# Kernel optimization log

Hardware: AMD Instinct MI355X
Metric: run time of the kernel (lower is better)

## Reference

```python
import jax, jax.numpy as jnp
import numpy as np

N_EMB = 1024
HEAD_SIZE = 128


def setup_inputs() -> dict:
    key = jax.random.key(0)
    k1, k2, k3, k4 = jax.random.split(key, 4)
    B, T = 8, 4096
    x = jax.random.normal(k1, (B, T, N_EMB), dtype=jnp.float32)
    # nn.Linear(n_emb, head_size, bias=False) weights have shape [head_size, n_emb]
    s = 1.0 / np.sqrt(N_EMB)
    Wq = jax.random.uniform(k2, (HEAD_SIZE, N_EMB), jnp.float32, -s, s)
    Wk = jax.random.uniform(k3, (HEAD_SIZE, N_EMB), jnp.float32, -s, s)
    Wv = jax.random.uniform(k4, (HEAD_SIZE, N_EMB), jnp.float32, -s, s)
    return {"x": x, "Wq": Wq, "Wk": Wk, "Wv": Wv}


def reference(x, Wq, Wk, Wv):
    # x: [B, T, C]; W*: [H, C]
    B, T, C = x.shape
    H = Wq.shape[0]
    q = jnp.einsum('btc,hc->bth', x, Wq)
    k = jnp.einsum('btc,hc->bth', x, Wk)
    v = jnp.einsum('btc,hc->bth', x, Wv)
    scale = H ** -0.5
    wei = jnp.einsum('bth,bsh->bts', q, k) * scale  # [B, T, T]
    # causal mask: position t attends to s <= t
    causal = jnp.arange(T)[:, None] >= jnp.arange(T)[None, :]
    wei = jnp.where(causal, wei, -jnp.inf)
    wei = jax.nn.softmax(wei, axis=-1)
    # dropout treated as identity (eval mode)
    out = jnp.einsum('bts,bsh->bth', wei, v)  # [B, T, H]
    return out
```

## Files before the change

### kernel.cpp

```cpp
#include <hip/hip_runtime.h>
#include <hip/hip_bf16.h>

typedef __bf16 bf16_t;
typedef __attribute__((ext_vector_type(8))) __bf16 bf16x8;
typedef __attribute__((ext_vector_type(4))) __bf16 bf16x4;
typedef __attribute__((ext_vector_type(4))) float f32x4;

#define MFMA16(a, b, c) __builtin_amdgcn_mfma_f32_16x16x32_bf16((a), (b), (c), 0, 0, 0)

__device__ __forceinline__ void gload_lds16(const void* g, void* l) {
    __builtin_amdgcn_global_load_lds(
        (const __attribute__((address_space(1))) void*)g,
        (__attribute__((address_space(3))) void*)l, 16, 0, 0);
}

__global__ __launch_bounds__(256, 3) void proj_qkv(
    const float* __restrict__ X,
    const float* __restrict__ W0, const float* __restrict__ W1, const float* __restrict__ W2,
    bf16_t* __restrict__ O0, bf16_t* __restrict__ O1, bf16_t* __restrict__ O2)
{
    __shared__ __align__(16) char As[128 * 128];
    __shared__ __align__(16) char Bs[128 * 128];

    const int tid = threadIdx.x;
    const int wid = tid >> 6;
    const int lane = tid & 63;
    const int l15 = lane & 15, l4 = lane >> 4;
    const int wr = wid >> 1, wc = wid & 1;
    const int m0 = blockIdx.x * 128;

    const float* W = (blockIdx.y == 0) ? W0 : (blockIdx.y == 1 ? W1 : W2);

    const int r0 = tid >> 4;
    const int kq = tid & 15;
    const int swz = ((r0 & 7) << 4);

    f32x4 acc[4][4] = {};
    float4 xr[8];

    #pragma unroll
    for (int i = 0; i < 8; ++i)
        xr[i] = *(const float4*)(X + (size_t)(m0 + r0 + i * 16) * 1024 + kq * 4);

    for (int ks = 0; ks < 16; ++ks) {
        const int kb = ks * 64;
        #pragma unroll
        for (int i = 0; i < 8; ++i) {
            const int r = r0 + i * 16;
            bf16x4 av; av[0] = (bf16_t)xr[i].x; av[1] = (bf16_t)xr[i].y;
            av[2] = (bf16_t)xr[i].z; av[3] = (bf16_t)xr[i].w;
            *(bf16x4*)(As + r * 128 + ((kq * 8) ^ swz)) = av;
        }
        #pragma unroll
        for (int i = 0; i < 8; ++i) {
            const int r = r0 + i * 16;
            float4 wa = *(const float4*)(W + (size_t)r * 1024 + kb + kq * 4);
            bf16x4 wv; wv[0] = (bf16_t)wa.x; wv[1] = (bf16_t)wa.y;
            wv[2] = (bf16_t)wa.z; wv[3] = (bf16_t)wa.w;
            *(bf16x4*)(Bs + r * 128 + ((kq * 8) ^ swz)) = wv;
        }
        __syncthreads();
        if (ks < 15) {
            #pragma unroll
            for (int i = 0; i < 8; ++i)
                xr[i] = *(const float4*)(X + (size_t)(m0 + r0 + i * 16) * 1024 + kb + 64 + kq * 4);
        }
        #pragma unroll
        for (int kk = 0; kk < 64; kk += 32) {
            const int kbyte = 2 * kk + 16 * l4;
            bf16x8 af[4], bfr[4];
            #pragma unroll
            for (int mi = 0; mi < 4; ++mi) {
                int r = wr * 64 + mi * 16 + l15;
                af[mi] = *(const bf16x8*)(As + r * 128 + (kbyte ^ ((r & 7) << 4)));
            }
            #pragma unroll
            for (int ni = 0; ni < 4; ++ni) {
                int r = wc * 64 + ni * 16 + l15;
                bfr[ni] = *(const bf16x8*)(Bs + r * 128 + (kbyte ^ ((r & 7) << 4)));
            }
            #pragma unroll
            for (int mi = 0; mi < 4; ++mi)
                #pragma unroll
                for (int ni = 0; ni < 4; ++ni)
                    acc[mi][ni] = MFMA16(af[mi], bfr[ni], acc[mi][ni]);
        }
        __syncthreads();
    }

    if (blockIdx.y < 2) {
        const float sc = (blockIdx.y == 0) ? 0.12751754816f : 1.0f;
        bf16_t* O = (blockIdx.y == 0) ? O0 : O1;
        #pragma unroll
        for (int mi = 0; mi < 4; ++mi)
            #pragma unroll
            for (int ni = 0; ni < 4; ++ni) {
                int row = m0 + wr * 64 + mi * 16 + l4 * 4;
                int col = wc * 64 + ni * 16 + l15;
                #pragma unroll
                for (int r = 0; r < 4; ++r)
                    O[(size_t)(row + r) * 128 + col] = (bf16_t)(acc[mi][ni][r] * sc);
            }
    } else {
        #pragma unroll
        for (int mi = 0; mi < 4; ++mi)
            #pragma unroll
            for (int ni = 0; ni < 4; ++ni) {
                int row0 = m0 + wr * 64 + mi * 16 + l4 * 4;
                int col = wc * 64 + ni * 16 + l15;
                int bb = row0 >> 12, t0 = row0 & 4095;
                bf16x4 pk;
                #pragma unroll
                for (int r = 0; r < 4; ++r) pk[r] = (bf16_t)acc[mi][ni][r];
                *(bf16x4*)(O2 + ((size_t)bb << 19) + (size_t)col * 4096 + t0) = pk;
            }
    }
}

__global__ __launch_bounds__(256, 2) void attn_fwd(
    const bf16_t* __restrict__ Qb, const bf16_t* __restrict__ Kb,
    const bf16_t* __restrict__ Vtg, float* __restrict__ out, int Bn)
{
    __shared__ __align__(16) char lds[81920];

    const int tid = threadIdx.x, wid = tid >> 6, lane = tid & 63;
    const int l15 = lane & 15, l4 = lane >> 4;
    const int pair = wid >> 1, qhalf = wid & 1;

    const int L = blockIdx.x;
    const int b = L % Bn;
    const int j = L / Bn;
    const int qt = (j < 32) ? j : 95 - j;
    const int q0 = qt << 6;
    const int steps = (qt >> 1) + 1;
    const int qw0 = q0 + 32 * qhalf;

    const size_t base = (size_t)b * 4096 * 128;

    bf16x8 aq[2][4];
    #pragma unroll
    for (int qs = 0; qs < 2; ++qs)
        #pragma unroll
        for (int kf = 0; kf < 4; ++kf)
            aq[qs][kf] = *(const bf16x8*)(Qb + base + (size_t)(qw0 + 16 * qs + l15) * 128 + 32 * kf + 8 * l4);

    float mx[2] = {-1e30f, -1e30f}, lsum[2] = {0.f, 0.f};
    f32x4 o[2][8] = {};

    char* Kbuf = lds + pair * 32768;
    char* Vbuf = Kbuf + 16384;
    char* Pw   = lds + 65536 + wid * 4096;
    char* stg  = lds + wid * 16384;

    const int sK_r = lane >> 4, sK_c = (lane & 15) << 4;
    const int sV_r = lane >> 3, sV_c = (lane & 7) << 4;

    auto stage = [&](int s) {
        const int t = 2 * s + pair;
        if (t * 64 > q0 + 63) return;
        const int kv0s = t << 6;
        if ((wid & 1) == 0) {
            #pragma unroll
            for (int i = 0; i < 16; ++i) {
                const int row = i * 4 + sK_r;
                const bf16_t* src = Kb + base + (size_t)(kv0s + row) * 128
                                    + ((sK_c ^ ((row & 7) << 4)) >> 1);
                gload_lds16(src, stg + i * 1024);
            }
        } else {
            #pragma unroll
            for (int i = 0; i < 16; ++i) {
                const int h = i * 8 + sV_r;
                const bf16_t* src = Vtg + base + (size_t)h * 4096 + kv0s
                                    + ((sV_c ^ ((h & 7) << 4)) >> 1);
                gload_lds16(src, stg + i * 1024);
            }
        }
    };

    stage(0);
    __syncthreads();

    for (int s = 0; s < steps; ++s) {
        const int tw = 2 * s + pair;
        const int kv0 = tw << 6;
        if (kv0 <= qw0 + 31) {
            f32x4 sa[2][4];
            #pragma unroll
            for (int qs = 0; qs < 2; ++qs)
                #pragma unroll
                for (int ni = 0; ni < 4; ++ni) sa[qs][ni] = (f32x4){0.f, 0.f, 0.f, 0.f};
            __builtin_amdgcn_s_setprio(1);
            #pragma unroll
            for (int kf = 0; kf < 4; ++kf) {
                const int kb = 64 * kf + 16 * l4;
                #pragma unroll
                for (int ni = 0; ni < 4; ++ni) {
                    const int krow = 16 * ni + l15;
                    bf16x8 ak = *(const bf16x8*)(Kbuf + krow * 256 + (kb ^ ((krow & 7) << 4)));
                    sa[0][ni] = MFMA16(ak, aq[0][kf], sa[0][ni]);
                    sa[1][ni] = MFMA16(ak, aq[1][kf], sa[1][ni]);
                }
            }
            __builtin_amdgcn_s_setprio(0);
            #pragma unroll
            for (int qs = 0; qs < 2; ++qs) {
                const int qg = qw0 + 16 * qs + l15;
                if (kv0 + 63 > qw0 + 16 * qs) {
                    #pragma unroll
                    for (int ni = 0; ni < 4; ++ni)
                        #pragma unroll
                        for (int r = 0; r < 4; ++r)
                            if (kv0 + 16 * ni + 4 * l4 + r > qg) sa[qs][ni][r] = -1e30f;
                }
                float tm = sa[qs][0][0];
                #pragma unroll
                for (int ni = 0; ni < 4; ++ni)
                    #pragma unroll
                    for (int r = 0; r < 4; ++r) tm = fmaxf(tm, sa[qs][ni][r]);
                tm = fmaxf(tm, __shfl_xor(tm, 16, 64));
                tm = fmaxf(tm, __shfl_xor(tm, 32, 64));
                const float mnew = fmaxf(mx[qs], tm);
                const float c = exp2f(mx[qs] - mnew);
                float ssum = 0.f;
                #pragma unroll
                for (int ni = 0; ni < 4; ++ni)
                    #pragma unroll
                    for (int r = 0; r < 4; ++r) {
                        float pv = exp2f(sa[qs][ni][r] - mnew);
                        sa[qs][ni][r] = pv;
                        ssum += pv;
                    }
                ssum += __shfl_xor(ssum, 16, 64);
                ssum += __shfl_xor(ssum, 32, 64);
                lsum[qs] = lsum[qs] * c + ssum;
                mx[qs] = mnew;
                #pragma unroll
                for (int mf = 0; mf < 8; ++mf) {
                    f32x4 t = o[qs][mf];
                    t[0] *= c; t[1] *= c; t[2] *= c; t[3] *= c;
                    o[qs][mf] = t;
                }
                const int rowb = (16 * qs + l15) * 128;
                const int swz = (l15 & 7) << 4;
                #pragma unroll
                for (int ni = 0; ni < 4; ++ni) {
                    bf16x4 pv;
                    pv[0] = (bf16_t)sa[qs][ni][0]; pv[1] = (bf16_t)sa[qs][ni][1];
                    pv[2] = (bf16_t)sa[qs][ni][2]; pv[3] = (bf16_t)sa[qs][ni][3];
                    *(bf16x4*)(Pw + rowb + ((32 * ni + 8 * l4) ^ swz)) = pv;
                }
            }
            const int swzp = (l15 & 7) << 4;
            __builtin_amdgcn_s_setprio(1);
            #pragma unroll
            for (int kfp = 0; kfp < 2; ++kfp) {
                const int kb = 64 * kfp + 16 * l4;
                bf16x8 p0 = *(const bf16x8*)(Pw + l15 * 128 + (kb ^ swzp));
                bf16x8 p1 = *(const bf16x8*)(Pw + (16 + l15) * 128 + (kb ^ swzp));
                #pragma unroll
                for (int mf = 0; mf < 8; ++mf) {
                    const int h = 16 * mf + l15;
                    bf16x8 av = *(const bf16x8*)(Vbuf + h * 128 + (kb ^ ((h & 7) << 4)));
                    o[0][mf] = MFMA16(av, p0, o[0][mf]);
                    o[1][mf] = MFMA16(av, p1, o[1][mf]);
                }
            }
            __builtin_amdgcn_s_setprio(0);
        }
        if (s + 1 < steps) {
            __syncthreads();
            stage(s + 1);
            __syncthreads();
        }
    }

    __syncthreads();
    if (wid >= 2) {
        char* dst = lds + (wid - 2) * 16384;
        #pragma unroll
        for (int qs = 0; qs < 2; ++qs)
            #pragma unroll
            for (int mf = 0; mf < 8; ++mf)
                *(f32x4*)(dst + (qs * 8 + mf) * 1024 + lane * 16) = o[qs][mf];
        f32x4 st; st[0] = mx[0]; st[1] = lsum[0]; st[2] = mx[1]; st[3] = lsum[1];
        *(f32x4*)(lds + 32768 + (wid - 2) * 1024 + lane * 16) = st;
    }
    __syncthreads();
    if (wid < 2) {
        char* srcO = lds + wid * 16384;
        f32x4 st = *(const f32x4*)(lds + 32768 + wid * 1024 + lane * 16);
        #pragma unroll
        for (int qs = 0; qs < 2; ++qs) {
            const float mB = st[2 * qs], lB = st[2 * qs + 1];
            const float mm = fmaxf(mx[qs], mB);
            const float a = exp2f(mx[qs] - mm), bb = exp2f(mB - mm);
            const float linv = 1.f / (lsum[qs] * a + lB * bb);
            const int qg = qw0 + 16 * qs + l15;
            float* op = out + ((size_t)b * 4096 + qg) * 128;
            #pragma unroll
            for (int mf = 0; mf < 8; ++mf) {
                f32x4 ob = *(const f32x4*)(srcO + (qs * 8 + mf) * 1024 + lane * 16);
                f32x4 r;
                #pragma unroll
                for (int e = 0; e < 4; ++e) r[e] = (o[qs][mf][e] * a + ob[e] * bb) * linv;
                *(f32x4*)(op + 16 * mf + 4 * l4) = r;
            }
        }
    }
}

extern "C" void kernel_launch(void* const* d_in, const int* in_sizes, int n_in,
                              void* d_out, int out_size, void* d_ws, size_t ws_size,
                              hipStream_t stream) {
    const float* X  = (const float*)d_in[0];
    const float* Wq = (const float*)d_in[1];
    const float* Wk = (const float*)d_in[2];
    const float* Wv = (const float*)d_in[3];
    float* out = (float*)d_out;

    const int M = in_sizes[0] / 1024;
    const int Bn = M / 4096;

    bf16_t* Qb  = (bf16_t*)d_ws;
    bf16_t* KbP = Qb + (size_t)M * 128;
    bf16_t* VtP = KbP + (size_t)M * 128;

    proj_qkv<<<dim3(M / 128, 3), 256, 0, stream>>>(X, Wq, Wk, Wv, Qb, KbP, VtP);
    attn_fwd<<<dim3(64 * Bn), 256, 0, stream>>>(Qb, KbP, VtP, out, Bn);
}
```

Before: 145.0 us.

## Restructure attention into per-wave split-KV with register K and double-buffered V

Each block now handles two 32-row query tiles, a short one and a long one, for load balance. The four waves split the KV tiles round-robin, each running its own online softmax. K is loaded straight into registers and prefetched one tile ahead, and V is staged per wave into double-buffered LDS with async loads, which removes the block-wide barriers inside the KV loop. The output rescale is skipped when no row max increases, and the four partial results are merged through LDS at the end. The cost is a larger four-way reduction, more register pressure from holding K in registers, and a hand-placed vmcnt wait that must match the number of loads issued.

```diff
diff --git a/kernel.cpp b/kernel.cpp
--- a/kernel.cpp
+++ b/kernel.cpp
@@ -121,192 +121,200 @@
     const bf16_t* __restrict__ Qb, const bf16_t* __restrict__ Kb,
     const bf16_t* __restrict__ Vtg, float* __restrict__ out, int Bn)
 {
-    __shared__ __align__(16) char lds[81920];
+    __shared__ __align__(16) char lds[73728];
 
     const int tid = threadIdx.x, wid = tid >> 6, lane = tid & 63;
     const int l15 = lane & 15, l4 = lane >> 4;
-    const int pair = wid >> 1, qhalf = wid & 1;
-
-    const int L = blockIdx.x;
-    const int b = L % Bn;
-    const int j = L / Bn;
-    const int qt = (j < 32) ? j : 95 - j;
-    const int q0 = qt << 6;
-    const int steps = (qt >> 1) + 1;
-    const int qw0 = q0 + 32 * qhalf;
+
+    const int blk = blockIdx.x;
+    const int b = blk % Bn;
+    const int j = blk / Bn;
 
     const size_t base = (size_t)b * 4096 * 128;
-
-    bf16x8 aq[2][4];
-    #pragma unroll
-    for (int qs = 0; qs < 2; ++qs)
-        #pragma unroll
-        for (int kf = 0; kf < 4; ++kf)
-            aq[qs][kf] = *(const bf16x8*)(Qb + base + (size_t)(qw0 + 16 * qs + l15) * 128 + 32 * kf + 8 * l4);
-
-    float mx[2] = {-1e30f, -1e30f}, lsum[2] = {0.f, 0.f};
-    f32x4 o[2][8] = {};
-
-    char* Kbuf = lds + pair * 32768;
-    char* Vbuf = Kbuf + 16384;
-    char* Pw   = lds + 65536 + wid * 4096;
-    char* stg  = lds + wid * 16384;
-
-    const int sK_r = lane >> 4, sK_c = (lane & 15) << 4;
-    const int sV_r = lane >> 3, sV_c = (lane & 7) << 4;
-
-    auto stage = [&](int s) {
-        const int t = 2 * s + pair;
-        if (t * 64 > q0 + 63) return;
-        const int kv0s = t << 6;
-        if ((wid & 1) == 0) {
-            #pragma unroll
-            for (int i = 0; i < 16; ++i) {
-                const int row = i * 4 + sK_r;
-                const bf16_t* src = Kb + base + (size_t)(kv0s + row) * 128
-                                    + ((sK_c ^ ((row & 7) << 4)) >> 1);
-                gload_lds16(src, stg + i * 1024);
-            }
-        } else {
-            #pragma unroll
-            for (int i = 0; i < 16; ++i) {
-                const int h = i * 8 + sV_r;
-                const bf16_t* src = Vtg + base + (size_t)h * 4096 + kv0s
-                                    + ((sV_c ^ ((h & 7) << 4)) >> 1);
-                gload_lds16(src, stg + i * 1024);
-            }
-        }
-    };
-
-    stage(0);
-    __syncthreads();
-
-    for (int s = 0; s < steps; ++s) {
-        const int tw = 2 * s + pair;
-        const int kv0 = tw << 6;
-        if (kv0 <= qw0 + 31) {
-            f32x4 sa[2][4];
+    const size_t baseVT = (size_t)b << 19;
+
+    char* Vw = lds + wid * 16384;
+    char* Pw = lds + 65536 + wid * 2048;
+
+    const int sh = lane >> 2;
+    const int skb = (lane & 3) * 8;
+
+    for (int seg = 0; seg < 2; ++seg) {
+        const int p = seg ? (127 - j) : j;
+        const int q0 = p << 5;
+        const int nt = (p >= wid) ? ((p - wid) >> 2) + 1 : 0;
+
+        bf16x8 aq[2][4];
+        #pragma unroll
+        for (int qs = 0; qs < 2; ++qs)
+            #pragma unroll
+            for (int kf = 0; kf < 4; ++kf)
+                aq[qs][kf] = *(const bf16x8*)(Qb + base
+                    + (size_t)(q0 + 16 * qs + l15) * 128 + 32 * kf + 8 * l4);
+
+        float mx[2] = {-1e30f, -1e30f}, lsum[2] = {0.f, 0.f};
+        f32x4 o[2][8] = {};
+        bf16x8 kreg[2][4];
+
+        auto stageV = [&](int i) {
+            const int kv0 = (wid + 4 * i) << 5;
+            char* dst = Vw + (i & 1) * 8192;
+            #pragma unroll
+            for (int c = 0; c < 8; ++c) {
+                const bf16_t* src = Vtg + baseVT + (size_t)(16 * c + sh) * 4096 + kv0 + skb;
+                gload_lds16(src, dst + c * 1024);
+            }
+        };
+        auto loadK = [&](int i) {
+            const int kv0 = (wid + 4 * i) << 5;
+            const bf16_t* kp = Kb + base + (size_t)(kv0 + l15) * 128 + 8 * l4;
+            #pragma unroll
+            for (int ni = 0; ni < 2; ++ni)
+                #pragma unroll
+                for (int kf = 0; kf < 4; ++kf)
+                    kreg[ni][kf] = *(const bf16x8*)(kp + (size_t)ni * 2048 + kf * 32);
+        };
+
+        if (nt > 0) { loadK(0); stageV(0); }
+
+        for (int i = 0; i < nt; ++i) {
+            const int lt = wid + 4 * i;
+            const int kv0 = lt << 5;
+
+            f32x4 sa[2][2];
             #pragma unroll
             for (int qs = 0; qs < 2; ++qs)
                 #pragma unroll
-                for (int ni = 0; ni < 4; ++ni) sa[qs][ni] = (f32x4){0.f, 0.f, 0.f, 0.f};
+                for (int ni = 0; ni < 2; ++ni) sa[qs][ni] = (f32x4){0.f, 0.f, 0.f, 0.f};
             __builtin_amdgcn_s_setprio(1);
             #pragma unroll
-            for (int kf = 0; kf < 4; ++kf) {
-                const int kb = 64 * kf + 16 * l4;
-                #pragma unroll
-                for (int ni = 0; ni < 4; ++ni) {
-                    const int krow = 16 * ni + l15;
-                    bf16x8 ak = *(const bf16x8*)(Kbuf + krow * 256 + (kb ^ ((krow & 7) << 4)));
-                    sa[0][ni] = MFMA16(ak, aq[0][kf], sa[0][ni]);
-                    sa[1][ni] = MFMA16(ak, aq[1][kf], sa[1][ni]);
-                }
-            }
+            for (int kf = 0; kf < 4; ++kf)
+                #pragma unroll
+                for (int ni = 0; ni < 2; ++ni) {
+                    sa[0][ni] = MFMA16(kreg[ni][kf], aq[0][kf], sa[0][ni]);
+                    sa[1][ni] = MFMA16(kreg[ni][kf], aq[1][kf], sa[1][ni]);
+                }
             __builtin_amdgcn_s_setprio(0);
-            #pragma unroll
-            for (int qs = 0; qs < 2; ++qs) {
-                const int qg = qw0 + 16 * qs + l15;
-                if (kv0 + 63 > qw0 + 16 * qs) {
-                    #pragma unroll
-                    for (int ni = 0; ni < 4; ++ni)
+
+            if (i + 1 < nt) loadK(i + 1);
+
+            if (lt == p) {
+                #pragma unroll
+                for (int qs = 0; qs < 2; ++qs) {
+                    const int qg = q0 + 16 * qs + l15;
+                    #pragma unroll
+                    for (int ni = 0; ni < 2; ++ni)
                         #pragma unroll
                         for (int r = 0; r < 4; ++r)
                             if (kv0 + 16 * ni + 4 * l4 + r > qg) sa[qs][ni][r] = -1e30f;
                 }
+            }
+
+            #pragma unroll
+            for (int qs = 0; qs < 2; ++qs) {
                 float tm = sa[qs][0][0];
                 #pragma unroll
-                for (int ni = 0; ni < 4; ++ni)
+                for (int ni = 0; ni < 2; ++ni)
                     #pragma unroll
                     for (int r = 0; r < 4; ++r) tm = fmaxf(tm, sa[qs][ni][r]);
                 tm = fmaxf(tm, __shfl_xor(tm, 16, 64));
                 tm = fmaxf(tm, __shfl_xor(tm, 32, 64));
-                const float mnew = fmaxf(mx[qs], tm);
-                const float c = exp2f(mx[qs] - mnew);
-                float ssum = 0.f;
-                #pragma unroll
-                for (int ni = 0; ni < 4; ++ni)
+                if (__any(tm > mx[qs])) {
+                    const float mnew = fmaxf(mx[qs], tm);
+                    const float c = exp2f(mx[qs] - mnew);
+                    lsum[qs] *= c;
+                    #pragma unroll
+                    for (int mf = 0; mf < 8; ++mf) {
+                        f32x4 t = o[qs][mf];
+                        t[0] *= c; t[1] *= c; t[2] *= c; t[3] *= c;
+                        o[qs][mf] = t;
+                    }
+                    mx[qs] = mnew;
+                }
+                float ss = 0.f;
+                #pragma unroll
+                for (int ni = 0; ni < 2; ++ni)
                     #pragma unroll
                     for (int r = 0; r < 4; ++r) {
-                        float pv = exp2f(sa[qs][ni][r] - mnew);
+                        float pv = exp2f(sa[qs][ni][r] - mx[qs]);
                         sa[qs][ni][r] = pv;
-                        ssum += pv;
+                        ss += pv;
                     }
-                ssum += __shfl_xor(ssum, 16, 64);
-                ssum += __shfl_xor(ssum, 32, 64);
-                lsum[qs] = lsum[qs] * c + ssum;
-                mx[qs] = mnew;
-                #pragma unroll
-                for (int mf = 0; mf < 8; ++mf) {
-                    f32x4 t = o[qs][mf];
-                    t[0] *= c; t[1] *= c; t[2] *= c; t[3] *= c;
-                    o[qs][mf] = t;
-                }
-                const int rowb = (16 * qs + l15) * 128;
-                const int swz = (l15 & 7) << 4;
-                #pragma unroll
-                for (int ni = 0; ni < 4; ++ni) {
+                ss += __shfl_xor(ss, 16, 64);
+                ss += __shfl_xor(ss, 32, 64);
+                lsum[qs] += ss;
+                #pragma unroll
+                for (int ni = 0; ni < 2; ++ni) {
                     bf16x4 pv;
                     pv[0] = (bf16_t)sa[qs][ni][0]; pv[1] = (bf16_t)sa[qs][ni][1];
                     pv[2] = (bf16_t)sa[qs][ni][2]; pv[3] = (bf16_t)sa[qs][ni][3];
-                    *(bf16x4*)(Pw + rowb + ((32 * ni + 8 * l4) ^ swz)) = pv;
-                }
-            }
-            const int swzp = (l15 & 7) << 4;
+                    *(bf16x4*)(Pw + (16 * qs + l15) * 64 + 32 * ni + 8 * l4) = pv;
+                }
+            }
+
+            __builtin_amdgcn_sched_barrier(0);
+            asm volatile("s_waitcnt vmcnt(8)" ::: "memory");
+            __builtin_amdgcn_sched_barrier(0);
+
+            char* Vbuf = Vw + (i & 1) * 8192;
+            bf16x8 pa0 = *(const bf16x8*)(Pw + l15 * 64 + 16 * l4);
+            bf16x8 pa1 = *(const bf16x8*)(Pw + (16 + l15) * 64 + 16 * l4);
             __builtin_amdgcn_s_setprio(1);
             #pragma unroll
-            for (int kfp = 0; kfp < 2; ++kfp) {
-                const int kb = 64 * kfp + 16 * l4;
-                bf16x8 p0 = *(const bf16x8*)(Pw + l15 * 128 + (kb ^ swzp));
-                bf16x8 p1 = *(const bf16x8*)(Pw + (16 + l15) * 128 + (kb ^ swzp));
-                #pragma unroll
-                for (int mf = 0; mf < 8; ++mf) {
-                    const int h = 16 * mf + l15;
-                    bf16x8 av = *(const bf16x8*)(Vbuf + h * 128 + (kb ^ ((h & 7) << 4)));
-                    o[0][mf] = MFMA16(av, p0, o[0][mf]);
-                    o[1][mf] = MFMA16(av, p1, o[1][mf]);
-                }
+            for (int mf = 0; mf < 8; ++mf) {
+                bf16x8 av = *(const bf16x8*)(Vbuf + (16 * mf + l15) * 64 + 16 * l4);
+                o[0][mf] = MFMA16(av, pa0, o[0][mf]);
+                o[1][mf] = MFMA16(av, pa1, o[1][mf]);
             }
             __builtin_amdgcn_s_setprio(0);
-        }
-        if (s + 1 < steps) {
-            __syncthreads();
-            stage(s + 1);
-            __syncthreads();
-        }
-    }
-
-    __syncthreads();
-    if (wid >= 2) {
-        char* dst = lds + (wid - 2) * 16384;
+
+            if (i + 1 < nt) stageV(i + 1);
+        }
+
+        asm volatile("s_waitcnt vmcnt(0)" ::: "memory");
+        __syncthreads();
         #pragma unroll
         for (int qs = 0; qs < 2; ++qs)
             #pragma unroll
             for (int mf = 0; mf < 8; ++mf)
-                *(f32x4*)(dst + (qs * 8 + mf) * 1024 + lane * 16) = o[qs][mf];
-        f32x4 st; st[0] = mx[0]; st[1] = lsum[0]; st[2] = mx[1]; st[3] = lsum[1];
-        *(f32x4*)(lds + 32768 + (wid - 2) * 1024 + lane * 16) = st;
-    }
-    __syncthreads();
-    if (wid < 2) {
-        char* srcO = lds + wid * 16384;
-        f32x4 st = *(const f32x4*)(lds + 32768 + wid * 1024 + lane * 16);
+                *(f32x4*)(lds + wid * 16384 + (qs * 8 + mf) * 1024 + lane * 16) = o[qs][mf];
+        if (l4 == 0) {
+            #pragma unroll
+            for (int qs = 0; qs < 2; ++qs)
+                *(float2*)(lds + 65536 + wid * 256 + (qs * 16 + l15) * 8)
+                    = make_float2(mx[qs], lsum[qs]);
+        }
+        __syncthreads();
         #pragma unroll
         for (int qs = 0; qs < 2; ++qs) {
-            const float mB = st[2 * qs], lB = st[2 * qs + 1];
-            const float mm = fmaxf(mx[qs], mB);
-            const float a = exp2f(mx[qs] - mm), bb = exp2f(mB - mm);
-            const float linv = 1.f / (lsum[qs] * a + lB * bb);
-            const int qg = qw0 + 16 * qs + l15;
-            float* op = out + ((size_t)b * 4096 + qg) * 128;
-            #pragma unroll
-            for (int mf = 0; mf < 8; ++mf) {
-                f32x4 ob = *(const f32x4*)(srcO + (qs * 8 + mf) * 1024 + lane * 16);
-                f32x4 r;
-                #pragma unroll
-                for (int e = 0; e < 4; ++e) r[e] = (o[qs][mf][e] * a + ob[e] * bb) * linv;
-                *(f32x4*)(op + 16 * mf + 4 * l4) = r;
-            }
-        }
+            float mw[4], lw[4];
+            #pragma unroll
+            for (int w = 0; w < 4; ++w) {
+                float2 st = *(const float2*)(lds + 65536 + w * 256 + (qs * 16 + l15) * 8);
+                mw[w] = st.x; lw[w] = st.y;
+            }
+            const float M = fmaxf(fmaxf(mw[0], mw[1]), fmaxf(mw[2], mw[3]));
+            float cw[4], L = 0.f;
+            #pragma unroll
+            for (int w = 0; w < 4; ++w) { cw[w] = exp2f(mw[w] - M); L += lw[w] * cw[w]; }
+            const float inv = 1.f / L;
+            #pragma unroll
+            for (int mm = 0; mm < 2; ++mm) {
+                const int mf = 2 * wid + mm;
+                f32x4 acc = (f32x4){0.f, 0.f, 0.f, 0.f};
+                #pragma unroll
+                for (int w = 0; w < 4; ++w) {
+                    f32x4 v = *(const f32x4*)(lds + w * 16384 + (qs * 8 + mf) * 1024 + lane * 16);
+                    #pragma unroll
+                    for (int e = 0; e < 4; ++e) acc[e] += v[e] * cw[w];
+                }
+                #pragma unroll
+                for (int e = 0; e < 4; ++e) acc[e] *= inv;
+                float* op = out + ((size_t)b * 4096 + q0 + 16 * qs + l15) * 128 + 16 * mf + 4 * l4;
+                *(f32x4*)op = acc;
+            }
+        }
+        __syncthreads();
     }
 }
 
```

Result: faster. 139.7 us (-3.6%).
